# Kernel tuning notes

Hardware: AMD Instinct MI355X
Metric: run time of the kernel (lower is better)

## Reference

```python
import jax, jax.numpy as jnp
import numpy as np

GROUPS = 8
HEADS = 8
EPS = 1e-5


def setup_inputs() -> dict:
    key = jax.random.key(0)
    ks = jax.random.split(key, 4)
    B, C, T = 4, 512, 2048
    x = jax.random.normal(ks[0], (B, C, T), dtype=jnp.float32)
    gn_w = jnp.ones((C,), dtype=jnp.float32)
    gn_b = jnp.zeros((C,), dtype=jnp.float32)
    qkv_w = jax.random.normal(ks[1], (3 * C, C), dtype=jnp.float32) * (1.0 / np.sqrt(C))
    qkv_b = jnp.zeros((3 * C,), dtype=jnp.float32)
    proj_w = jax.random.normal(ks[2], (C, C), dtype=jnp.float32) * (1.0 / np.sqrt(C))
    proj_b = jnp.zeros((C,), dtype=jnp.float32)
    return {"x": x, "gn_w": gn_w, "gn_b": gn_b, "qkv_w": qkv_w,
            "qkv_b": qkv_b, "proj_w": proj_w, "proj_b": proj_b}


def reference(x, gn_w, gn_b, qkv_w, qkv_b, proj_w, proj_b):
    b, c, t = x.shape
    # GroupNorm over (channels_in_group, T)
    xg = x.reshape(b, GROUPS, c // GROUPS, t)
    mean = xg.mean(axis=(2, 3), keepdims=True)
    var = xg.var(axis=(2, 3), keepdims=True)
    h = ((xg - mean) * jax.lax.rsqrt(var + EPS)).reshape(b, c, t)
    h = h * gn_w[None, :, None] + gn_b[None, :, None]
    # 1x1 conv qkv: [b, 3c, t]
    qkv = jnp.einsum('oc,bct->bot', qkv_w, h) + qkv_b[None, :, None]
    # split into heads: legacy layout [b*H, 3*ch, t] -> q,k,v each [b*H, ch, t]
    ch = c // HEADS
    qkv = qkv.reshape(b * HEADS, 3 * ch, t)
    q, k, v = qkv[:, :ch], qkv[:, ch:2 * ch], qkv[:, 2 * ch:]
    scale = 1.0 / np.sqrt(np.sqrt(ch))
    weight = jnp.einsum('bct,bcs->bts', q * scale, k * scale)  # [bH, t, t]
    weight = jax.nn.softmax(weight.astype(jnp.float32), axis=-1).astype(q.dtype)
    a = jnp.einsum('bts,bcs->bct', weight, v).reshape(b, c, t)
    # 1x1 conv proj
    out = jnp.einsum('oc,bct->bot', proj_w, a) + proj_b[None, :, None]
    return x + out
```

## Files before the change

### kernel.cpp

```cpp
#include <hip/hip_runtime.h>


typedef __attribute__((ext_vector_type(8))) short short8;
typedef __attribute__((ext_vector_type(4))) float f32x4;
typedef __attribute__((ext_vector_type(16))) float f32x16;

#define T_DIM 2048
#define C_DIM 512
#define B_DIM 4

__device__ __forceinline__ float bf2f(ushort u) {
  union { unsigned int i; float f; } x; x.i = ((unsigned int)u) << 16; return x.f;
}
__device__ __forceinline__ ushort f2bf(float f) {
  union { float f; unsigned int i; } x; x.f = f;
  unsigned int i = x.i;
  return (ushort)((i + 0x7FFFu + ((i >> 16) & 1u)) >> 16);
}
__device__ __forceinline__ unsigned int cvtpk_bf16(float lo, float hi) {
  unsigned int r;
  asm("v_cvt_pk_bf16_f32 %0, %1, %2" : "=v"(r) : "v"(lo), "v"(hi));
  return r;
}
__device__ __forceinline__ float exp2_raw(float x) {
  float r;
  asm("v_exp_f32 %0, %1" : "=v"(r) : "v"(x));
  return r;
}
__device__ __forceinline__ void gl_lds16(const ushort* g, const ushort* l) {
  __builtin_amdgcn_global_load_lds(
      (const __attribute__((address_space(1))) unsigned int*)g,
      (__attribute__((address_space(3))) unsigned int*)l, 16, 0, 0);
}

#define KT_SCALE 0.1803368801f

__global__ __launch_bounds__(256) void prep_kernel(
    const float* __restrict__ qkv_w, ushort* __restrict__ wq,
    const float* __restrict__ proj_w, ushort* __restrict__ wp,
    const float* __restrict__ x, float2* __restrict__ part) {
  const int bi = blockIdx.x;
  const int tid = threadIdx.x;
  if (bi < 1024) {
    const float* s = (bi < 768) ? qkv_w : proj_w;
    ushort* d = (bi < 768) ? wq : wp;
    int i = ((bi < 768) ? bi : bi - 768) * 256 + tid;
    float4 v = ((const float4*)s)[i];
    ushort4 o;
    o.x = f2bf(v.x); o.y = f2bf(v.y); o.z = f2bf(v.z); o.w = f2bf(v.w);
    ((ushort4*)d)[i] = o;
    return;
  }
  const int pb = bi - 1024;
  const float4* p4 = (const float4*)x + (size_t)pb * 2048;
  float s = 0.f, ss = 0.f;
#pragma unroll
  for (int i = 0; i < 8; i++) {
    float4 v = p4[tid + i * 256];
    s += v.x + v.y + v.z + v.w;
    ss += v.x * v.x + v.y * v.y + v.z * v.z + v.w * v.w;
  }
  for (int off = 32; off; off >>= 1) {
    s += __shfl_xor(s, off, 64);
    ss += __shfl_xor(ss, off, 64);
  }
  __shared__ float rbuf[8];
  int w = tid >> 6, lane = tid & 63;
  if (lane == 0) { rbuf[w * 2] = s; rbuf[w * 2 + 1] = ss; }
  __syncthreads();
  if (tid == 0) {
    float S = 0.f, SS = 0.f;
#pragma unroll
    for (int i = 0; i < 4; i++) { S += rbuf[2 * i]; SS += rbuf[2 * i + 1]; }
    part[pb] = make_float2(S, SS);
  }
}

__global__ __launch_bounds__(256) void gn_apply_t_kernel(
    const float* __restrict__ x, const float* __restrict__ gw,
    const float* __restrict__ gb, const float2* __restrict__ part,
    ushort* __restrict__ ht) {
  __shared__ ushort tile[64][66];
  __shared__ float sst[2];
  const int b = blockIdx.z, gy = blockIdx.y, c0 = gy * 64, t0 = blockIdx.x * 64;
  const int tid = threadIdx.x;
  if (tid < 64) {
    float s = 0.f, ss = 0.f;
    if (tid < 16) {
      float2 p = part[(b * 8 + gy) * 16 + tid];
      s = p.x; ss = p.y;
    }
    for (int off = 8; off; off >>= 1) {
      s += __shfl_xor(s, off, 64);
      ss += __shfl_xor(ss, off, 64);
    }
    if (tid == 0) {
      float mean = s * (1.f / 131072.f);
      float var = ss * (1.f / 131072.f) - mean * mean;
      sst[0] = mean;
      sst[1] = rsqrtf(var + 1e-5f);
    }
  }
  __syncthreads();
  const float mean = sst[0], rstd = sst[1];
  {
    const int cc = tid >> 2, tc = (tid & 3) * 16;
    const int c = c0 + cc;
    float sc = rstd * gw[c];
    float bb = gb[c] - mean * sc;
    const float4* src = (const float4*)(x + ((size_t)b * 512 + c) * T_DIM + t0 + tc);
    unsigned int* dst = (unsigned int*)&tile[cc][tc];
#pragma unroll
    for (int q = 0; q < 4; q++) {
      float4 v = src[q];
      float a0 = v.x * sc + bb, a1 = v.y * sc + bb;
      float a2 = v.z * sc + bb, a3 = v.w * sc + bb;
      dst[2 * q] = (unsigned int)f2bf(a0) | ((unsigned int)f2bf(a1) << 16);
      dst[2 * q + 1] = (unsigned int)f2bf(a2) | ((unsigned int)f2bf(a3) << 16);
    }
  }
  __syncthreads();
  {
    const int tt = tid >> 2, ch = (tid & 3) * 16;
    union { uint4 v4[2]; ushort u[16]; } z;
#pragma unroll
    for (int j = 0; j < 16; j++) z.u[j] = tile[ch + j][tt];
    ushort* dst = ht + ((size_t)b * T_DIM + t0 + tt) * 512 + c0 + ch;
    *(uint4*)dst = z.v4[0];
    *(uint4*)(dst + 8) = z.v4[1];
  }
}

template <int MODE>
__global__ __launch_bounds__(256, 3) void gemm_bt_kernel(
    const ushort* __restrict__ Wb, const ushort* __restrict__ Bt,
    const float* __restrict__ bias, const float* __restrict__ xres,
    ushort* __restrict__ outb, float* __restrict__ outf,
    ushort* __restrict__ ktp, int M) {
  __shared__ ushort As[128 * 64];
  __shared__ ushort Bs[128 * 64];
  const int b = blockIdx.z;
  const int t0 = blockIdx.x * 128, o0 = blockIdx.y * 128;
  const int tid = threadIdx.x, lane = tid & 63, w = tid >> 6;
  const int li = lane & 15, g = lane >> 4;
  const int wm = (w >> 1) * 64, wn = (w & 1) * 64;
  const int r8 = tid >> 3, bl = tid & 7;
  const ushort* Bbase = Bt + (size_t)b * T_DIM * 512;

  f32x4 acc[4][4];
#pragma unroll
  for (int m = 0; m < 4; m++)
#pragma unroll
    for (int n = 0; n < 4; n++) acc[m][n] = (f32x4){0.f, 0.f, 0.f, 0.f};

  for (int ks = 0; ks < 8; ks++) {
    const int k0 = ks * 64;
#pragma unroll
    for (int i = 0; i < 4; i++) {
      int row = i * 32 + r8;
      int sb = (bl ^ (row & 7)) << 3;
      gl_lds16(Wb + (size_t)(o0 + row) * 512 + k0 + sb, As + row * 64 + bl * 8);
      gl_lds16(Bbase + (size_t)(t0 + row) * 512 + k0 + sb, Bs + row * 64 + bl * 8);
    }
    __syncthreads();
#pragma unroll
    for (int kk = 0; kk < 2; kk++) {
      short8 af[4], bf[4];
#pragma unroll
      for (int m = 0; m < 4; m++)
        af[m] = *(const short8*)&As[(wm + m * 16 + li) * 64 +
                                    (((kk * 4 + g) ^ (li & 7)) << 3)];
#pragma unroll
      for (int n = 0; n < 4; n++)
        bf[n] = *(const short8*)&Bs[(wn + n * 16 + li) * 64 +
                                    (((kk * 4 + g) ^ (li & 7)) << 3)];
      __builtin_amdgcn_s_setprio(1);
#pragma unroll
      for (int m = 0; m < 4; m++)
#pragma unroll
        for (int n = 0; n < 4; n++)
          acc[m][n] = __builtin_amdgcn_mfma_f32_16x16x32_bf16(af[m], bf[n],
                                                              acc[m][n], 0, 0, 0);
      __builtin_amdgcn_s_setprio(0);
    }
    __syncthreads();
  }

  size_t obase = (size_t)b * M * T_DIM;
#pragma unroll
  for (int m = 0; m < 4; m++) {
    const int om = o0 + wm + m * 16;
    bool isK = false;
    int head = 0, rem0 = 0;
    if (MODE == 0) {
      head = om / 192;
      rem0 = om - head * 192;
      isK = (rem0 >= 64 && rem0 < 128);
    }
    if (MODE == 0 && isK) {
      const int d0 = rem0 - 64 + g * 4;
      const size_t ktbase = (size_t)(b * 8 + head) * T_DIM;
      float bv0 = bias[om + g * 4 + 0];
      float bv1 = bias[om + g * 4 + 1];
      float bv2 = bias[om + g * 4 + 2];
      float bv3 = bias[om + g * 4 + 3];
#pragma unroll
      for (int n = 0; n < 4; n++) {
        int t = t0 + wn + n * 16 + li;
        ushort4 kv;
        kv.x = f2bf(KT_SCALE * (acc[m][n][0] + bv0));
        kv.y = f2bf(KT_SCALE * (acc[m][n][1] + bv1));
        kv.z = f2bf(KT_SCALE * (acc[m][n][2] + bv2));
        kv.w = f2bf(KT_SCALE * (acc[m][n][3] + bv3));
        *(ushort4*)(ktp + (ktbase + t) * 64 + d0) = kv;
      }
    } else {
#pragma unroll
      for (int r = 0; r < 4; r++) {
        int o = om + g * 4 + r;
        float bv = bias[o];
#pragma unroll
        for (int n = 0; n < 4; n++) {
          int t = t0 + wn + n * 16 + li;
          float v = acc[m][n][r] + bv;
          size_t idx = obase + (size_t)o * T_DIM + t;
          if (MODE == 0) outb[idx] = f2bf(v);
          else outf[idx] = v + xres[idx];
        }
      }
    }
  }
}

__global__ __launch_bounds__(256, 4) void attn_part_kernel(
    const ushort* __restrict__ qkv, const ushort* __restrict__ Ktg,
    ushort* __restrict__ opart, float* __restrict__ lpart) {
  __shared__ ushort SH[16384];
  const int bh = blockIdx.x, b = bh >> 3, hh = bh & 7;
  const int ttile = blockIdx.y;
  const int t0 = ttile * 128;
  const int sq = blockIdx.z;
  const int tid = threadIdx.x, lane = tid & 63, w = tid >> 6;
  const int tl = lane & 31, hi = lane >> 5;
  const size_t base = ((size_t)b * 1536 + hh * 192) * (size_t)T_DIM;
  const ushort* Qp = qkv + base;
  const ushort* Vp = qkv + base + (size_t)128 * T_DIM + sq * 512;
  const ushort* Kp = Ktg + (size_t)bh * T_DIM * 64 + (size_t)sq * 512 * 64;
  const int tcol = t0 + w * 32 + tl;

  short8 qb[4];
#pragma unroll
  for (int kc = 0; kc < 4; kc++) {
    union { short8 s; ushort u[8]; } tmp;
#pragma unroll
    for (int j = 0; j < 8; j++)
      tmp.u[j] = Qp[(size_t)(kc * 16 + hi * 8 + j) * T_DIM + tcol];
    qb[kc] = tmp.s;
  }

  const int srow = lane >> 3;
  const int sblk = (lane & 7) ^ srow;

  const ushort* kg = Kp + (size_t)(w * 16 + srow) * 64 + sblk * 8;
  const ushort* vg = Vp + (size_t)(w * 16 + srow) * T_DIM + sblk * 8;
  const int ldW = w * 1024;

  f32x16 zv;
#pragma unroll
  for (int r = 0; r < 16; r++) zv[r] = 0.f;
  f32x16 oacc0, oacc1;
#pragma unroll
  for (int r = 0; r < 16; r++) { oacc0[r] = 0.f; oacc1[r] = 0.f; }
  float lsum = 0.f;

  gl_lds16(kg, SH + ldW);
  gl_lds16(kg + 512, SH + ldW + 512);
  gl_lds16(vg, SH + 8192 + ldW);
  gl_lds16(vg + 8 * T_DIM, SH + 8192 + ldW + 512);
  kg += 4096;
  vg += 64;

#define CHUNK(BUF, PF)                                                        \
  {                                                                           \
    __syncthreads();                                                          \
    if (PF) {                                                                 \
      gl_lds16(kg, SH + ((BUF) ^ 1) * 4096 + ldW);                            \
      gl_lds16(kg + 512, SH + ((BUF) ^ 1) * 4096 + ldW + 512);                \
      gl_lds16(vg, SH + 8192 + ((BUF) ^ 1) * 4096 + ldW);                     \
      gl_lds16(vg + 8 * T_DIM, SH + 8192 + ((BUF) ^ 1) * 4096 + ldW + 512);   \
      kg += 4096;                                                             \
      vg += 64;                                                               \
    }                                                                         \
    const ushort* kb = SH + (BUF) * 4096;                                     \
    const ushort* vb = SH + 8192 + (BUF) * 4096;                              \
    f32x16 s0, s1;                                                            \
    __builtin_amdgcn_s_setprio(1);                                            \
    _Pragma("unroll") for (int kc = 0; kc < 4; kc++) {                        \
      const int bo = (((kc * 2 + hi) ^ (tl & 7)) << 3);                       \
      short8 ak0 = *(const short8*)&kb[tl * 64 + bo];                         \
      short8 ak1 = *(const short8*)&kb[(32 + tl) * 64 + bo];                  \
      s0 = __builtin_amdgcn_mfma_f32_32x32x16_bf16(ak0, qb[kc],               \
                                                   kc == 0 ? zv : s0, 0, 0, 0);\
      s1 = __builtin_amdgcn_mfma_f32_32x32x16_bf16(ak1, qb[kc],               \
                                                   kc == 0 ? zv : s1, 0, 0, 0);\
    }                                                                         \
    __builtin_amdgcn_s_setprio(0);                                            \
    _Pragma("unroll") for (int r = 0; r < 16; r++) {                          \
      s0[r] = exp2_raw(s0[r]);                                                \
      s1[r] = exp2_raw(s1[r]);                                                \
    }                                                                         \
    {                                                                         \
      float a0 = (s0[0] + s0[1]) + (s0[2] + s0[3]);                           \
      float a1 = (s0[4] + s0[5]) + (s0[6] + s0[7]);                           \
      float a2 = (s0[8] + s0[9]) + (s0[10] + s0[11]);                         \
      float a3 = (s0[12] + s0[13]) + (s0[14] + s0[15]);                       \
      float b0 = (s1[0] + s1[1]) + (s1[2] + s1[3]);                           \
      float b1 = (s1[4] + s1[5]) + (s1[6] + s1[7]);                           \
      float b2 = (s1[8] + s1[9]) + (s1[10] + s1[11]);                         \
      float b3 = (s1[12] + s1[13]) + (s1[14] + s1[15]);                       \
      lsum += ((a0 + a1) + (a2 + a3)) + ((b0 + b1) + (b2 + b3));              \
    }                                                                         \
    unsigned int pw[2][8];                                                    \
    _Pragma("unroll") for (int p = 0; p < 8; p++) {                           \
      pw[0][p] = cvtpk_bf16(s0[2 * p], s0[2 * p + 1]);                        \
      pw[1][p] = cvtpk_bf16(s1[2 * p], s1[2 * p + 1]);                        \
    }                                                                         \
    short8 bp[4];                                                             \
    _Pragma("unroll") for (int kc = 0; kc < 4; kc++) {                        \
      const int n = kc >> 1, q = (kc & 1) * 4;                                \
      union { short8 s; unsigned int wv[4]; } bu;                             \
      _Pragma("unroll") for (int h = 0; h < 2; h++) {                         \
        unsigned int P0 = pw[n][q + h];                                       \
        unsigned int P1 = pw[n][q + 2 + h];                                   \
        asm volatile("v_permlane32_swap_b32 %0, %1" : "+v"(P0), "+v"(P1));    \
        bu.wv[h] = P0;                                                        \
        bu.wv[2 + h] = P1;                                                    \
      }                                                                       \
      bp[kc] = bu.s;                                                          \
    }                                                                         \
    __builtin_amdgcn_s_setprio(1);                                            \
    _Pragma("unroll") for (int kc = 0; kc < 4; kc++) {                        \
      const int bo = (((kc * 2 + hi) ^ (tl & 7)) << 3);                       \
      short8 av0 = *(const short8*)&vb[tl * 64 + bo];                         \
      short8 av1 = *(const short8*)&vb[(32 + tl) * 64 + bo];                  \
      oacc0 = __builtin_amdgcn_mfma_f32_32x32x16_bf16(av0, bp[kc], oacc0,     \
                                                      0, 0, 0);               \
      oacc1 = __builtin_amdgcn_mfma_f32_32x32x16_bf16(av1, bp[kc], oacc1,     \
                                                      0, 0, 0);               \
    }                                                                         \
    __builtin_amdgcn_s_setprio(0);                                            \
  }

  for (int cc = 0; cc < 4; cc++) {
    CHUNK(0, true);
    CHUNK(1, cc < 3);
  }
#undef CHUNK

  const int pidx = (bh * 16 + ttile) * 4 + sq;
  ushort* op = opart + (size_t)pidx * 8192;
#pragma unroll
  for (int r = 0; r < 16; r++) {
    int crow = (r & 3) + 8 * (r >> 2) + 4 * hi;
    op[crow * 128 + w * 32 + tl] = f2bf(oacc0[r]);
    op[(32 + crow) * 128 + w * 32 + tl] = f2bf(oacc1[r]);
  }
  float lrow = lsum + __shfl_xor(lsum, 32);
  if (hi == 0) lpart[(size_t)pidx * 128 + w * 32 + tl] = lrow;
}

__global__ __launch_bounds__(256) void combine_kernel(
    const ushort* __restrict__ opart, const float* __restrict__ lpart,
    ushort* __restrict__ at) {
  __shared__ float invl[128];
  __shared__ ushort tile[128][66];
  const int bh = blockIdx.x, ttile = blockIdx.y, b = bh >> 3, hh = bh & 7;
  const int tid = threadIdx.x;
  const size_t pb = (size_t)(bh * 16 + ttile) * 4;
  const float* l0 = lpart + pb * 128;
  if (tid < 128)
    invl[tid] = 1.f / (l0[tid] + l0[128 + tid] + l0[256 + tid] + l0[384 + tid]);
  __syncthreads();
  {
    const int c = tid & 63, seg = tid >> 6;
    const ushort* r0 = opart + pb * 8192 + c * 128 + seg * 32;
    union { uint4 v[4]; ushort u[32]; } x0, x1, x2, x3;
#pragma unroll
    for (int j = 0; j < 4; j++) {
      x0.v[j] = *(const uint4*)(r0 + j * 8);
      x1.v[j] = *(const uint4*)(r0 + 8192 + j * 8);
      x2.v[j] = *(const uint4*)(r0 + 16384 + j * 8);
      x3.v[j] = *(const uint4*)(r0 + 24576 + j * 8);
    }
#pragma unroll
    for (int j = 0; j < 32; j++) {
      int t = seg * 32 + j;
      float v = (bf2f(x0.u[j]) + bf2f(x1.u[j])) + (bf2f(x2.u[j]) + bf2f(x3.u[j]));
      tile[t][c] = f2bf(v * invl[t]);
    }
  }
  __syncthreads();
  {
    const int t = tid >> 1, ch = (tid & 1) * 32;
    union { uint4 v[4]; ushort u[32]; } z;
#pragma unroll
    for (int j = 0; j < 32; j++) z.u[j] = tile[t][ch + j];
    uint4* dst = (uint4*)(at + ((size_t)b * T_DIM + ttile * 128 + t) * 512 +
                          hh * 64 + ch);
#pragma unroll
    for (int j = 0; j < 4; j++) dst[j] = z.v[j];
  }
}

extern "C" void kernel_launch(void* const* d_in, const int* in_sizes, int n_in,
                              void* d_out, int out_size, void* d_ws,
                              size_t ws_size, hipStream_t stream) {
  const float* x = (const float*)d_in[0];
  const float* gn_w = (const float*)d_in[1];
  const float* gn_b = (const float*)d_in[2];
  const float* qkv_w = (const float*)d_in[3];
  const float* qkv_b = (const float*)d_in[4];
  const float* proj_w = (const float*)d_in[5];
  const float* proj_b = (const float*)d_in[6];
  float* out = (float*)d_out;

  char* ws = (char*)d_ws;
  float2* part = (float2*)ws;
  ushort* ht_bf = (ushort*)(ws + 8192);
  ushort* at_bf = ht_bf;
  ushort* qkv_bf = (ushort*)(ws + 8192 + 8388608);
  ushort* wq_bf = (ushort*)(ws + 8192 + 8388608 + 25165824);
  ushort* wp_bf = (ushort*)(ws + 8192 + 8388608 + 25165824 + 1572864);
  ushort* kt_bf = (ushort*)(ws + 8192 + 8388608 + 25165824 + 1572864 + 524288);
  ushort* op_bf = (ushort*)(ws + 8192 + 8388608 + 25165824 + 1572864 + 524288 +
                            8388608);
  float* lp_f = (float*)(ws + 8192 + 8388608 + 25165824 + 1572864 + 524288 +
                         8388608 + 33554432);

  prep_kernel<<<1536, 256, 0, stream>>>(qkv_w, wq_bf, proj_w, wp_bf, x, part);
  gn_apply_t_kernel<<<dim3(32, 8, 4), 256, 0, stream>>>(x, gn_w, gn_b, part, ht_bf);
  gemm_bt_kernel<0><<<dim3(16, 12, 4), 256, 0, stream>>>(
      wq_bf, ht_bf, qkv_b, nullptr, qkv_bf, nullptr, kt_bf, 1536);
  attn_part_kernel<<<dim3(32, 16, 4), 256, 0, stream>>>(qkv_bf, kt_bf, op_bf, lp_f);
  combine_kernel<<<dim3(32, 16), 256, 0, stream>>>(op_bf, lp_f, at_bf);
  gemm_bt_kernel<1><<<dim3(16, 4, 4), 256, 0, stream>>>(
      wp_bf, at_bf, proj_b, x, nullptr, out, nullptr, 512);
}
```

Measured before the change: 107.1 us.

## Halve attention key splits and shrink proj GEMM M-tile for more blocks

The attention kernel now splits the key dimension into two halves of 1024 instead of four quarters of 512. This halves the partial outputs written and read by the combine kernel, at the cost of fewer blocks in the attention grid (1024 instead of 2048). The GEMM kernel gains an MF template parameter for the M-tile height. The projection GEMM uses 64-row tiles, doubling its grid to 512 blocks to fill more CUs.

```diff
diff --git a/kernel.cpp b/kernel.cpp
--- a/kernel.cpp
+++ b/kernel.cpp
@@ -131,25 +131,25 @@
   }
 }
 
-template <int MODE>
+template <int MODE, int MF>
 __global__ __launch_bounds__(256, 3) void gemm_bt_kernel(
     const ushort* __restrict__ Wb, const ushort* __restrict__ Bt,
     const float* __restrict__ bias, const float* __restrict__ xres,
     ushort* __restrict__ outb, float* __restrict__ outf,
     ushort* __restrict__ ktp, int M) {
-  __shared__ ushort As[128 * 64];
+  __shared__ ushort As[MF * 32 * 64];
   __shared__ ushort Bs[128 * 64];
   const int b = blockIdx.z;
-  const int t0 = blockIdx.x * 128, o0 = blockIdx.y * 128;
+  const int t0 = blockIdx.x * 128, o0 = blockIdx.y * (MF * 32);
   const int tid = threadIdx.x, lane = tid & 63, w = tid >> 6;
   const int li = lane & 15, g = lane >> 4;
-  const int wm = (w >> 1) * 64, wn = (w & 1) * 64;
+  const int wm = (w >> 1) * (MF * 16), wn = (w & 1) * 64;
   const int r8 = tid >> 3, bl = tid & 7;
   const ushort* Bbase = Bt + (size_t)b * T_DIM * 512;
 
-  f32x4 acc[4][4];
-#pragma unroll
-  for (int m = 0; m < 4; m++)
+  f32x4 acc[MF][4];
+#pragma unroll
+  for (int m = 0; m < MF; m++)
 #pragma unroll
     for (int n = 0; n < 4; n++) acc[m][n] = (f32x4){0.f, 0.f, 0.f, 0.f};
 
@@ -159,15 +159,16 @@
     for (int i = 0; i < 4; i++) {
       int row = i * 32 + r8;
       int sb = (bl ^ (row & 7)) << 3;
-      gl_lds16(Wb + (size_t)(o0 + row) * 512 + k0 + sb, As + row * 64 + bl * 8);
+      if (i < MF)
+        gl_lds16(Wb + (size_t)(o0 + row) * 512 + k0 + sb, As + row * 64 + bl * 8);
       gl_lds16(Bbase + (size_t)(t0 + row) * 512 + k0 + sb, Bs + row * 64 + bl * 8);
     }
     __syncthreads();
 #pragma unroll
     for (int kk = 0; kk < 2; kk++) {
-      short8 af[4], bf[4];
-#pragma unroll
-      for (int m = 0; m < 4; m++)
+      short8 af[MF], bf[4];
+#pragma unroll
+      for (int m = 0; m < MF; m++)
         af[m] = *(const short8*)&As[(wm + m * 16 + li) * 64 +
                                     (((kk * 4 + g) ^ (li & 7)) << 3)];
 #pragma unroll
@@ -176,7 +177,7 @@
                                     (((kk * 4 + g) ^ (li & 7)) << 3)];
       __builtin_amdgcn_s_setprio(1);
 #pragma unroll
-      for (int m = 0; m < 4; m++)
+      for (int m = 0; m < MF; m++)
 #pragma unroll
         for (int n = 0; n < 4; n++)
           acc[m][n] = __builtin_amdgcn_mfma_f32_16x16x32_bf16(af[m], bf[n],
@@ -188,7 +189,7 @@
 
   size_t obase = (size_t)b * M * T_DIM;
 #pragma unroll
-  for (int m = 0; m < 4; m++) {
+  for (int m = 0; m < MF; m++) {
     const int om = o0 + wm + m * 16;
     bool isK = false;
     int head = 0, rem0 = 0;
@@ -239,13 +240,13 @@
   const int bh = blockIdx.x, b = bh >> 3, hh = bh & 7;
   const int ttile = blockIdx.y;
   const int t0 = ttile * 128;
-  const int sq = blockIdx.z;
+  const int shalf = blockIdx.z;
   const int tid = threadIdx.x, lane = tid & 63, w = tid >> 6;
   const int tl = lane & 31, hi = lane >> 5;
   const size_t base = ((size_t)b * 1536 + hh * 192) * (size_t)T_DIM;
   const ushort* Qp = qkv + base;
-  const ushort* Vp = qkv + base + (size_t)128 * T_DIM + sq * 512;
-  const ushort* Kp = Ktg + (size_t)bh * T_DIM * 64 + (size_t)sq * 512 * 64;
+  const ushort* Vp = qkv + base + (size_t)128 * T_DIM + shalf * 1024;
+  const ushort* Kp = Ktg + (size_t)bh * T_DIM * 64 + (size_t)shalf * 1024 * 64;
   const int tcol = t0 + w * 32 + tl;
 
   short8 qb[4];
@@ -351,13 +352,13 @@
     __builtin_amdgcn_s_setprio(0);                                            \
   }
 
-  for (int cc = 0; cc < 4; cc++) {
+  for (int cc = 0; cc < 8; cc++) {
     CHUNK(0, true);
-    CHUNK(1, cc < 3);
+    CHUNK(1, cc < 7);
   }
 #undef CHUNK
 
-  const int pidx = (bh * 16 + ttile) * 4 + sq;
+  const int pidx = (bh * 16 + ttile) * 2 + shalf;
   ushort* op = opart + (size_t)pidx * 8192;
 #pragma unroll
   for (int r = 0; r < 16; r++) {
@@ -376,27 +377,23 @@
   __shared__ ushort tile[128][66];
   const int bh = blockIdx.x, ttile = blockIdx.y, b = bh >> 3, hh = bh & 7;
   const int tid = threadIdx.x;
-  const size_t pb = (size_t)(bh * 16 + ttile) * 4;
+  const size_t pb = (size_t)(bh * 16 + ttile) * 2;
   const float* l0 = lpart + pb * 128;
-  if (tid < 128)
-    invl[tid] = 1.f / (l0[tid] + l0[128 + tid] + l0[256 + tid] + l0[384 + tid]);
+  if (tid < 128) invl[tid] = 1.f / (l0[tid] + l0[128 + tid]);
   __syncthreads();
   {
     const int c = tid & 63, seg = tid >> 6;
     const ushort* r0 = opart + pb * 8192 + c * 128 + seg * 32;
-    union { uint4 v[4]; ushort u[32]; } x0, x1, x2, x3;
+    union { uint4 v[4]; ushort u[32]; } x0, x1;
 #pragma unroll
     for (int j = 0; j < 4; j++) {
       x0.v[j] = *(const uint4*)(r0 + j * 8);
       x1.v[j] = *(const uint4*)(r0 + 8192 + j * 8);
-      x2.v[j] = *(const uint4*)(r0 + 16384 + j * 8);
-      x3.v[j] = *(const uint4*)(r0 + 24576 + j * 8);
     }
 #pragma unroll
     for (int j = 0; j < 32; j++) {
       int t = seg * 32 + j;
-      float v = (bf2f(x0.u[j]) + bf2f(x1.u[j])) + (bf2f(x2.u[j]) + bf2f(x3.u[j]));
-      tile[t][c] = f2bf(v * invl[t]);
+      tile[t][c] = f2bf((bf2f(x0.u[j]) + bf2f(x1.u[j])) * invl[t]);
     }
   }
   __syncthreads();
@@ -435,14 +432,14 @@
   ushort* op_bf = (ushort*)(ws + 8192 + 8388608 + 25165824 + 1572864 + 524288 +
                             8388608);
   float* lp_f = (float*)(ws + 8192 + 8388608 + 25165824 + 1572864 + 524288 +
-                         8388608 + 33554432);
+                         8388608 + 16777216);
 
   prep_kernel<<<1536, 256, 0, stream>>>(qkv_w, wq_bf, proj_w, wp_bf, x, part);
   gn_apply_t_kernel<<<dim3(32, 8, 4), 256, 0, stream>>>(x, gn_w, gn_b, part, ht_bf);
-  gemm_bt_kernel<0><<<dim3(16, 12, 4), 256, 0, stream>>>(
+  gemm_bt_kernel<0, 4><<<dim3(16, 12, 4), 256, 0, stream>>>(
       wq_bf, ht_bf, qkv_b, nullptr, qkv_bf, nullptr, kt_bf, 1536);
-  attn_part_kernel<<<dim3(32, 16, 4), 256, 0, stream>>>(qkv_bf, kt_bf, op_bf, lp_f);
+  attn_part_kernel<<<dim3(32, 16, 2), 256, 0, stream>>>(qkv_bf, kt_bf, op_bf, lp_f);
   combine_kernel<<<dim3(32, 16), 256, 0, stream>>>(op_bf, lp_f, at_bf);
-  gemm_bt_kernel<1><<<dim3(16, 4, 4), 256, 0, stream>>>(
+  gemm_bt_kernel<1, 2><<<dim3(16, 8, 4), 256, 0, stream>>>(
       wp_bf, at_bf, proj_b, x, nullptr, out, nullptr, 512);
 }
```

After: 96.97 us. 1.1x faster.
